# Kernel tuning notes

Measured on AMD Instinct MI355X. Metric: run time of the kernel, lower is better.

The kernel has to match this reference:

```python
import jax, jax.numpy as jnp
import numpy as np

N_NODES = 50000
N_EDGES = 600000
CHANNELS = 128
HEADS = 8


def setup_inputs() -> dict:
    key = jax.random.key(0)
    k1, k2, k3 = jax.random.split(key, 3)
    x = jax.random.normal(k1, (N_NODES, CHANNELS), dtype=jnp.float32)
    edge_index = jax.random.randint(k2, (2, N_EDGES), 0, N_NODES, dtype=jnp.int32)
    att = jax.random.normal(k3, (HEADS, 2 * (CHANNELS // HEADS)), dtype=jnp.float32)
    return {"x": x, "edge_index": edge_index, "att": att}


def reference(x, edge_index, att):
    # x: [N, C], edge_index: [2, E], att: [H, 2*D] with D = C // H
    src, dst = edge_index[0], edge_index[1]
    n = x.shape[0]
    h = att.shape[0]
    d = att.shape[1] // 2

    x_src = x[src].reshape(-1, h, d)   # [E, H, D]
    x_dst = x[dst].reshape(-1, h, d)   # [E, H, D]

    # (cat([x_src, x_dst]) * att).sum(-1) == x_src @ att[:, :D] + x_dst @ att[:, D:]
    a_src, a_dst = att[:, :d], att[:, d:]
    alpha = jnp.einsum('ehd,hd->eh', x_src, a_src) + jnp.einsum('ehd,hd->eh', x_dst, a_dst)
    alpha = jnp.where(alpha >= 0, alpha, 0.2 * alpha)  # LeakyReLU(0.2)

    # segment softmax over dst; torch scatter_reduce amax includes the zero init,
    # so the per-node max is max(segment_max, 0)
    seg_max = jax.ops.segment_max(alpha, dst, num_segments=n)  # [N, H]
    seg_max = jnp.maximum(seg_max, 0.0)
    alpha = jnp.exp(alpha - seg_max[dst])
    seg_sum = jax.ops.segment_sum(alpha, dst, num_segments=n)  # [N, H]
    alpha = alpha / jnp.maximum(seg_sum[dst], 1e-10)

    # weighted scatter-add of source features
    weighted = x_src * alpha[..., None]                        # [E, H, D]
    out = jax.ops.segment_sum(weighted, dst, num_segments=n)   # [N, H, D]
    return out.reshape(n, -1)
```

## Files before the change

kernel.cpp:

```cpp
#include <hip/hip_runtime.h>

#define N_NODES  50000
#define N_EDGES  600000
#define CHANNELS 128
#define HEADS    8
#define HEAD_DIM 16
#define CAP      64
#define CSTRIDE  16

#define PREP_BLOCK 256
#define EPT        8
#define SCAT_TH    (N_EDGES / EPT)
#define SCAT_VB    ((SCAT_TH + PREP_BLOCK - 1) / PREP_BLOCK)
#define LOGIT_VB   ((N_NODES * (CHANNELS / 4)) / PREP_BLOCK)
#define WPB        4

__global__ void prep_kernel(const float* __restrict__ x,
                            const float* __restrict__ att,
                            const int*   __restrict__ src,
                            const int*   __restrict__ dst,
                            int*            __restrict__ cursor,
                            unsigned short* __restrict__ bucket,
                            float*          __restrict__ ls8,
                            float*          __restrict__ ld8,
                            unsigned short* __restrict__ xb) {
    int b = blockIdx.x;
    if (b < SCAT_VB) {
        int t = b * PREP_BLOCK + threadIdx.x;
        if (t < SCAT_TH) {
            int dd[EPT], ss[EPT], pp[EPT];
#pragma unroll
            for (int k = 0; k < EPT; ++k) {
                int e = t + k * SCAT_TH;
                dd[k] = dst[e];
                ss[k] = src[e];
            }
#pragma unroll
            for (int k = 0; k < EPT; ++k)
                pp[k] = atomicAdd(&cursor[dd[k] * CSTRIDE], 1);
#pragma unroll
            for (int k = 0; k < EPT; ++k)
                if (pp[k] < CAP)
                    bucket[(size_t)dd[k] * CAP + pp[k]] = (unsigned short)ss[k];
        }
    } else {
        int gid = (b - SCAT_VB) * PREP_BLOCK + threadIdx.x;
        int n  = gid >> 5;
        int c4 = gid & 31;
        int h  = c4 >> 2;
        int j4 = c4 & 3;

        float4 v = ((const float4*)x)[gid];

        unsigned int ux = __float_as_uint(v.x), uy = __float_as_uint(v.y);
        unsigned int uz = __float_as_uint(v.z), uw = __float_as_uint(v.w);
        ushort4 pk;
        pk.x = (unsigned short)((ux + 0x7FFFu + ((ux >> 16) & 1u)) >> 16);
        pk.y = (unsigned short)((uy + 0x7FFFu + ((uy >> 16) & 1u)) >> 16);
        pk.z = (unsigned short)((uz + 0x7FFFu + ((uz >> 16) & 1u)) >> 16);
        pk.w = (unsigned short)((uw + 0x7FFFu + ((uw >> 16) & 1u)) >> 16);
        ((ushort4*)xb)[gid] = pk;

        float4 as4 = ((const float4*)att)[h * 8 + j4];
        float4 ad4 = ((const float4*)att)[h * 8 + 4 + j4];
        float ts = v.x * as4.x + v.y * as4.y + v.z * as4.z + v.w * as4.w;
        float td = v.x * ad4.x + v.y * ad4.y + v.z * ad4.z + v.w * ad4.w;
        ts += __shfl_xor(ts, 1, 4); ts += __shfl_xor(ts, 2, 4);
        td += __shfl_xor(td, 1, 4); td += __shfl_xor(td, 2, 4);
        if (j4 == 0) {
            ls8[n * HEADS + h] = ts;
            ld8[n * HEADS + h] = td;
        }
    }
}

__global__ void fused_gat_kernel(const unsigned short* __restrict__ xb,
                                 const float* __restrict__ ls8,
                                 const float* __restrict__ ld8,
                                 const int*   __restrict__ cursor,
                                 const unsigned short* __restrict__ bucket,
                                 float*       __restrict__ out) {
    __shared__ float s_p[WPB * CAP * HEADS];

    int wave = threadIdx.x >> 6;
    int lane = threadIdx.x & 63;
    int n = blockIdx.x * WPB + wave;
    if (n >= N_NODES) return;
    int h = lane >> 3;
    int j = lane & 7;
    int r   = lane >> 5;
    int l32 = lane & 31;
    int h2  = l32 >> 2;

    int   cnt_raw = cursor[n * CSTRIDE];
    int   myidx   = (int)bucket[(size_t)n * CAP + lane];
    float ldst    = ld8[n * HEADS + h];
    int cnt = (cnt_raw > CAP) ? CAP : cnt_raw;

    float* sp = s_p + wave * (CAP * HEADS);

    float av[8];
    float mymax = -1e30f;
#pragma unroll
    for (int k = 0; k < 8; ++k) {
        int i = j + 8 * k;
        av[k] = -1e30f;
        if (i < cnt) {
            int   s  = __shfl(myidx, i);
            float lg = ls8[s * HEADS + h] + ldst;
            float a  = (lg >= 0.0f) ? lg : 0.2f * lg;
            av[k] = a;
            mymax = fmaxf(mymax, a);
        }
    }
#pragma unroll
    for (int o = 4; o >= 1; o >>= 1) mymax = fmaxf(mymax, __shfl_xor(mymax, o, 8));
    float m = fmaxf(mymax, 0.0f);

    float myl = 0.0f;
#pragma unroll
    for (int k = 0; k < 8; ++k) {
        int i = j + 8 * k;
        if (i < cnt) {
            float p = __expf(av[k] - m);
            sp[i * HEADS + h] = p;
            myl += p;
        }
    }
#pragma unroll
    for (int o = 4; o >= 1; o >>= 1) myl += __shfl_xor(myl, o, 8);

#define LP(k) ( ((const uint2*)(xb + (size_t)__shfl(myidx, ((2*(k)+r) < cnt) ? (2*(k)+r) : 0) * CHANNELS))[l32] )
    uint2 q[8];
#pragma unroll
    for (int k = 0; k < 8; ++k) q[k] = LP(k);

    float a0 = 0.f, a1 = 0.f, a2 = 0.f, a3 = 0.f;
    int npair = (cnt + 1) >> 1;
    int k = 0;
    for (; k + 4 <= npair; k += 4) {
#pragma unroll
        for (int u = 0; u < 4; ++u) {
            int e2 = 2 * (k + u) + r;
            float p = (e2 < cnt) ? sp[e2 * HEADS + h2] : 0.0f;
            uint2 qq = q[u];
            a0 += p * __uint_as_float(qq.x << 16);
            a1 += p * __uint_as_float(qq.x & 0xFFFF0000u);
            a2 += p * __uint_as_float(qq.y << 16);
            a3 += p * __uint_as_float(qq.y & 0xFFFF0000u);
        }
#pragma unroll
        for (int u = 0; u < 4; ++u) q[u] = q[u + 4];
#pragma unroll
        for (int u = 0; u < 4; ++u) q[u + 4] = LP(k + 8 + u);
    }
    for (; k < npair; ++k) {
        int e2 = 2 * k + r;
        float p = (e2 < cnt) ? sp[e2 * HEADS + h2] : 0.0f;
        uint2 qq = q[0];
        a0 += p * __uint_as_float(qq.x << 16);
        a1 += p * __uint_as_float(qq.x & 0xFFFF0000u);
        a2 += p * __uint_as_float(qq.y << 16);
        a3 += p * __uint_as_float(qq.y & 0xFFFF0000u);
#pragma unroll
        for (int u = 0; u < 7; ++u) q[u] = q[u + 1];
    }
#undef LP

    a0 += __shfl_xor(a0, 32);
    a1 += __shfl_xor(a1, 32);
    a2 += __shfl_xor(a2, 32);
    a3 += __shfl_xor(a3, 32);

    float denom = __shfl(myl, h2 * 8);
    float inv = 1.0f / fmaxf(denom, 1e-10f);

    if (lane < 32) {
        float4 o4 = make_float4(a0 * inv, a1 * inv, a2 * inv, a3 * inv);
        ((float4*)(out + (size_t)n * CHANNELS))[l32] = o4;
    }
}

extern "C" void kernel_launch(void* const* d_in, const int* in_sizes, int n_in,
                              void* d_out, int out_size, void* d_ws, size_t ws_size,
                              hipStream_t stream) {
    const float* x   = (const float*)d_in[0];
    const int*   ei  = (const int*)  d_in[1];
    const float* att = (const float*)d_in[2];
    const int* src = ei;
    const int* dst = ei + N_EDGES;
    float* out = (float*)d_out;

    int*            cursor = (int*)d_ws;
    unsigned short* bucket = (unsigned short*)(cursor + (size_t)N_NODES * CSTRIDE);
    float*          ls8    = (float*)(bucket + (size_t)N_NODES * CAP);
    float*          ld8    = ls8 + (size_t)N_NODES * HEADS;
    unsigned short* xb     = (unsigned short*)(ld8 + (size_t)N_NODES * HEADS);

    hipMemsetAsync(cursor, 0, sizeof(int) * (size_t)N_NODES * CSTRIDE, stream);

    prep_kernel<<<SCAT_VB + LOGIT_VB, PREP_BLOCK, 0, stream>>>(
        x, att, src, dst, cursor, bucket, ls8, ld8, xb);

    {
        int grid = (N_NODES + WPB - 1) / WPB;
        fused_gat_kernel<<<grid, 64 * WPB, 0, stream>>>(
            xb, ls8, ld8, cursor, bucket, out);
    }
}
```

Before: 147.2 us.

## Replace global-atomic edge bucketing with two-level binned counting sort

Edges are no longer bucketed by one global atomic per edge on a padded cursor array. Instead a per-chunk histogram over 256 destination-node bins runs alongside the logit/bf16 prep, a scan builds per-chunk offsets, and edges are scattered into per-bin segments as packed (src, dst) words. A final per-bin kernel fills each node's bucket using LDS atomics. This aims to remove global atomic contention and the cursor memset, in exchange for three extra kernel launches, more passes over the edge data, and a low-parallelism bucket stage. The fixed per-bin capacity of 2816 can silently drop edges if one bin overflows.

```diff
diff --git a/kernel.cpp b/kernel.cpp
--- a/kernel.cpp
+++ b/kernel.cpp
@@ -6,45 +6,42 @@
 #define HEADS    8
 #define HEAD_DIM 16
 #define CAP      64
-#define CSTRIDE  16
-
-#define PREP_BLOCK 256
-#define EPT        8
-#define SCAT_TH    (N_EDGES / EPT)
-#define SCAT_VB    ((SCAT_TH + PREP_BLOCK - 1) / PREP_BLOCK)
-#define LOGIT_VB   ((N_NODES * (CHANNELS / 4)) / PREP_BLOCK)
-#define WPB        4
-
-__global__ void prep_kernel(const float* __restrict__ x,
-                            const float* __restrict__ att,
-                            const int*   __restrict__ src,
-                            const int*   __restrict__ dst,
-                            int*            __restrict__ cursor,
-                            unsigned short* __restrict__ bucket,
-                            float*          __restrict__ ls8,
-                            float*          __restrict__ ld8,
-                            unsigned short* __restrict__ xb) {
+
+#define NBINS    256
+#define CHUNK_E  1024
+#define NCHUNK   ((N_EDGES + CHUNK_E - 1) / CHUNK_E)
+#define SEGCAP   2816
+#define NPB      200
+
+#define LOGIT_VB ((N_NODES * (CHANNELS / 4)) / 256)
+#define WPB      4
+
+__global__ void hist_logit_kernel(const float* __restrict__ x,
+                                  const float* __restrict__ att,
+                                  const int*   __restrict__ dst,
+                                  int*            __restrict__ hist,
+                                  float*          __restrict__ ls8,
+                                  float*          __restrict__ ld8,
+                                  unsigned short* __restrict__ xb) {
     int b = blockIdx.x;
-    if (b < SCAT_VB) {
-        int t = b * PREP_BLOCK + threadIdx.x;
-        if (t < SCAT_TH) {
-            int dd[EPT], ss[EPT], pp[EPT];
-#pragma unroll
-            for (int k = 0; k < EPT; ++k) {
-                int e = t + k * SCAT_TH;
-                dd[k] = dst[e];
-                ss[k] = src[e];
+    int t = threadIdx.x;
+    if (b < NCHUNK) {
+        __shared__ int lh[NBINS];
+        lh[t] = 0;
+        __syncthreads();
+        int base = b * CHUNK_E;
+#pragma unroll
+        for (int k = 0; k < 4; ++k) {
+            int e = base + t + k * 256;
+            if (e < N_EDGES) {
+                unsigned bin = (unsigned)(dst[e] * NBINS) / N_NODES;
+                atomicAdd(&lh[bin], 1);
             }
-#pragma unroll
-            for (int k = 0; k < EPT; ++k)
-                pp[k] = atomicAdd(&cursor[dd[k] * CSTRIDE], 1);
-#pragma unroll
-            for (int k = 0; k < EPT; ++k)
-                if (pp[k] < CAP)
-                    bucket[(size_t)dd[k] * CAP + pp[k]] = (unsigned short)ss[k];
-        }
+        }
+        __syncthreads();
+        hist[b * NBINS + t] = lh[t];
     } else {
-        int gid = (b - SCAT_VB) * PREP_BLOCK + threadIdx.x;
+        int gid = (b - NCHUNK) * 256 + t;
         int n  = gid >> 5;
         int c4 = gid & 31;
         int h  = c4 >> 2;
@@ -74,6 +71,75 @@
     }
 }
 
+__global__ void scan_kernel(const int* __restrict__ hist,
+                            int* __restrict__ offm,
+                            int* __restrict__ bincnt) {
+    __shared__ int lds[1024];
+    int bin = blockIdx.x;
+    int t = threadIdx.x;
+    int v = (t < NCHUNK) ? hist[t * NBINS + bin] : 0;
+    lds[t] = v;
+    __syncthreads();
+    for (int off = 1; off < 1024; off <<= 1) {
+        int u = (t >= off) ? lds[t - off] : 0;
+        __syncthreads();
+        lds[t] += u;
+        __syncthreads();
+    }
+    if (t < NCHUNK) offm[t * NBINS + bin] = lds[t] - v;
+    if (t == 1023) bincnt[bin] = lds[t];
+}
+
+__global__ void binscatter_kernel(const int* __restrict__ src,
+                                  const int* __restrict__ dst,
+                                  const int* __restrict__ offm,
+                                  unsigned*  __restrict__ ebuf) {
+    __shared__ int loff[NBINS];
+    __shared__ int lcnt[NBINS];
+    int b = blockIdx.x;
+    int t = threadIdx.x;
+    loff[t] = offm[b * NBINS + t];
+    lcnt[t] = 0;
+    __syncthreads();
+    int base = b * CHUNK_E;
+#pragma unroll
+    for (int k = 0; k < 4; ++k) {
+        int e = base + t + k * 256;
+        if (e < N_EDGES) {
+            int d = dst[e];
+            int s = src[e];
+            unsigned bin = (unsigned)(d * NBINS) / N_NODES;
+            int r = atomicAdd(&lcnt[bin], 1) + loff[bin];
+            if (r < SEGCAP)
+                ebuf[(size_t)bin * SEGCAP + r] = (unsigned)s | ((unsigned)d << 16);
+        }
+    }
+}
+
+__global__ void bucket_kernel(const unsigned* __restrict__ ebuf,
+                              const int*      __restrict__ bincnt,
+                              int*            __restrict__ cursor,
+                              unsigned short* __restrict__ bucket) {
+    __shared__ int lcnt[NPB];
+    int b = blockIdx.x;
+    int t = threadIdx.x;
+    int n0 = (b * N_NODES + NBINS - 1) / NBINS;
+    int n1 = ((b + 1) * N_NODES + NBINS - 1) / NBINS;
+    int nn = n1 - n0;
+    if (t < NPB) lcnt[t] = 0;
+    __syncthreads();
+    int cnt = min(bincnt[b], SEGCAP);
+    for (int i = t; i < cnt; i += 256) {
+        unsigned rec = ebuf[(size_t)b * SEGCAP + i];
+        int s = (int)(rec & 0xFFFFu);
+        int d = (int)(rec >> 16);
+        int pos = atomicAdd(&lcnt[d - n0], 1);
+        if (pos < CAP) bucket[(size_t)d * CAP + pos] = (unsigned short)s;
+    }
+    __syncthreads();
+    if (t < nn) cursor[n0 + t] = lcnt[t];
+}
+
 __global__ void fused_gat_kernel(const unsigned short* __restrict__ xb,
                                  const float* __restrict__ ls8,
                                  const float* __restrict__ ld8,
@@ -92,7 +158,7 @@
     int l32 = lane & 31;
     int h2  = l32 >> 2;
 
-    int   cnt_raw = cursor[n * CSTRIDE];
+    int   cnt_raw = cursor[n];
     int   myidx   = (int)bucket[(size_t)n * CAP + lane];
     float ldst    = ld8[n * HEADS + h];
     int cnt = (cnt_raw > CAP) ? CAP : cnt_raw;
@@ -191,20 +257,21 @@
     const int* dst = ei + N_EDGES;
     float* out = (float*)d_out;
 
-    int*            cursor = (int*)d_ws;
-    unsigned short* bucket = (unsigned short*)(cursor + (size_t)N_NODES * CSTRIDE);
+    int*            hist   = (int*)d_ws;
+    int*            offm   = hist + (size_t)NCHUNK * NBINS;
+    int*            bincnt = offm + (size_t)NCHUNK * NBINS;
+    unsigned*       ebuf   = (unsigned*)(bincnt + NBINS);
+    int*            cursor = (int*)(ebuf + (size_t)NBINS * SEGCAP);
+    unsigned short* bucket = (unsigned short*)(cursor + N_NODES);
     float*          ls8    = (float*)(bucket + (size_t)N_NODES * CAP);
     float*          ld8    = ls8 + (size_t)N_NODES * HEADS;
     unsigned short* xb     = (unsigned short*)(ld8 + (size_t)N_NODES * HEADS);
 
-    hipMemsetAsync(cursor, 0, sizeof(int) * (size_t)N_NODES * CSTRIDE, stream);
-
-    prep_kernel<<<SCAT_VB + LOGIT_VB, PREP_BLOCK, 0, stream>>>(
-        x, att, src, dst, cursor, bucket, ls8, ld8, xb);
-
-    {
-        int grid = (N_NODES + WPB - 1) / WPB;
-        fused_gat_kernel<<<grid, 64 * WPB, 0, stream>>>(
-            xb, ls8, ld8, cursor, bucket, out);
-    }
-}
+    hist_logit_kernel<<<NCHUNK + LOGIT_VB, 256, 0, stream>>>(
+        x, att, dst, hist, ls8, ld8, xb);
+    scan_kernel<<<NBINS, 1024, 0, stream>>>(hist, offm, bincnt);
+    binscatter_kernel<<<NCHUNK, 256, 0, stream>>>(src, dst, offm, ebuf);
+    bucket_kernel<<<NBINS, 256, 0, stream>>>(ebuf, bincnt, cursor, bucket);
+    fused_gat_kernel<<<(N_NODES + WPB - 1) / WPB, 64 * WPB, 0, stream>>>(
+        xb, ls8, ld8, cursor, bucket, out);
+}
```

New measurement: 138.5 us. 1.06x faster.
